# Kernel tuning notes

Measured on AMD Instinct MI355X. Metric: run time of the kernel, lower is better.

The kernel has to match this reference:

```python
import jax, jax.numpy as jnp
import numpy as np

N, F_IN, F_OUT, H = 4096, 128, 64, 8
NEG_SLOPE = 0.2

def leaky_relu(x):
    return jnp.where(x >= 0, x, NEG_SLOPE * x)

def setup_inputs() -> dict:
    key = jax.random.key(0)
    k = jax.random.split(key, 6)
    x = jax.random.normal(k[0], (N, F_IN), dtype=jnp.float32)
    conn = jax.random.uniform(k[1], (N, N)) < 0.1
    conn = conn | jnp.eye(N, dtype=bool)
    topology = jnp.where(conn, 0.0, -1e9).astype(jnp.float32)
    proj = jax.random.normal(k[2], (H, F_IN, F_OUT), dtype=jnp.float32) * (1.0 / np.sqrt(F_IN))
    score_src = jax.random.normal(k[3], (H, F_OUT), dtype=jnp.float32) * (1.0 / np.sqrt(F_OUT))
    score_dst = jax.random.normal(k[4], (H, F_OUT), dtype=jnp.float32) * (1.0 / np.sqrt(F_OUT))
    skip_w = jax.random.normal(k[5], (H * F_OUT, F_IN), dtype=jnp.float32) * (1.0 / np.sqrt(F_IN))
    return {"x": x, "topology": topology, "proj": proj,
            "score_src": score_src, "score_dst": score_dst, "skip_w": skip_w}

def reference(x, topology, proj, score_src, score_dst, skip_w):
    # dropout is identity at inference time
    # projected node features: [H, N, F_OUT]
    h = jnp.einsum('ni,hio->hno', x, proj)
    # additive attention scores (GAT): [H, N, 1] + [H, 1, N] -> [H, N, N]
    s_src = jnp.einsum('hno,ho->hn', h, score_src)
    s_dst = jnp.einsum('hno,ho->hn', h, score_dst)
    scores = leaky_relu(s_src[:, :, None] + s_dst[:, None, :])
    attn = jax.nn.softmax(scores + topology[None, :, :], axis=-1)  # [H, N, N]
    # aggregate neighbors, then transpose heads to [N, H, F_OUT]
    out = jnp.einsum('hij,hjo->iho', attn, h)
    # skip connection (F_OUT != F_IN -> projected skip)
    out = out + (x @ skip_w.T).reshape(N, H, F_OUT)
    # mean over heads (concat_heads=False), then LeakyReLU activation
    out = leaky_relu(jnp.mean(out, axis=1))  # [N, F_OUT]
    return out
```

## Files before the change

kernel.cpp:

```cpp
#include <hip/hip_runtime.h>
#include <hip/hip_bf16.h>

#define NN 4096
#define FIN 128
#define FOUT 64
#define NH 8
#define KS 4

typedef float f32x4 __attribute__((ext_vector_type(4)));
typedef _Float16 f16x8 __attribute__((ext_vector_type(8)));
typedef _Float16 h2 __attribute__((ext_vector_type(2)));
typedef unsigned long long u64;

static __device__ __forceinline__ h2 as_h2(unsigned u) { return __builtin_bit_cast(h2, u); }
static __device__ __forceinline__ unsigned as_u32(h2 v) { return __builtin_bit_cast(unsigned, v); }

static __device__ __forceinline__ u64 spread4(u64 x) {
    x = (x | (x << 24)) & 0x000000FF000000FFull;
    x = (x | (x << 12)) & 0x000F000F000F000Full;
    x = (x | (x << 6))  & 0x0303030303030303ull;
    x = (x | (x << 3))  & 0x1111111111111111ull;
    return x;
}

__global__ __launch_bounds__(256) void maskwc_kernel(
    const float* __restrict__ topo, u64* __restrict__ mb,
    const float* __restrict__ proj, const float* __restrict__ score_src,
    const float* __restrict__ score_dst, const float* __restrict__ skip_w,
    float* __restrict__ Wc) {
    const int tid = threadIdx.x;
    if (blockIdx.x < 2048) {
        const int wg = blockIdx.x * 4 + (tid >> 6);
        const int lane = tid & 63;
        const size_t base = (size_t)wg * 32;
        const float* tp = topo + base * 64 + lane * 4;
#pragma unroll
        for (int it = 0; it < 8; ++it) {
            float4 v = *(const float4*)(tp + it * 256);
            u64 b0 = __ballot(v.x > -0.5e9f);
            u64 b1 = __ballot(v.y > -0.5e9f);
            u64 b2 = __ballot(v.z > -0.5e9f);
            u64 b3 = __ballot(v.w > -0.5e9f);
            u64 wv[4];
#pragma unroll
            for (int g = 0; g < 4; ++g) {
                u64 x0 = spread4((b0 >> (16 * g)) & 0xFFFFu);
                u64 x1 = spread4((b1 >> (16 * g)) & 0xFFFFu);
                u64 x2 = spread4((b2 >> (16 * g)) & 0xFFFFu);
                u64 x3 = spread4((b3 >> (16 * g)) & 0xFFFFu);
                wv[g] = x0 | (x1 << 1) | (x2 << 2) | (x3 << 3);
            }
            if (lane == 0) {
                ulonglong2 s01; s01.x = wv[0]; s01.y = wv[1];
                ulonglong2 s23; s23.x = wv[2]; s23.y = wv[3];
                *(ulonglong2*)&mb[base + it * 4] = s01;
                *(ulonglong2*)&mb[base + it * 4 + 2] = s23;
            }
        }
        return;
    }
    int idx = (blockIdx.x - 2048) * 256 + tid;
    if (idx >= FIN * 80) return;
    int i = idx / 80, c = idx % 80;
    float v = 0.f;
    if (c < 16) {
        int h = c & 7;
        const float* w = (c < 8 ? score_src : score_dst) + h * FOUT;
        const float* p = proj + (size_t)h * FIN * FOUT + (size_t)i * FOUT;
        for (int f = 0; f < FOUT; ++f) v += p[f] * w[f];
    } else {
        int f = c - 16;
        for (int h = 0; h < NH; ++h) v += skip_w[(size_t)(h * FOUT + f) * FIN + i];
        v *= 0.125f;
    }
    Wc[i * 80 + c] = v;
}

__global__ __launch_bounds__(256) void scores_kernel(
    const float* __restrict__ x, const float* __restrict__ Wc,
    float* __restrict__ skipm, _Float16* __restrict__ Eh, _Float16* __restrict__ Fh,
    unsigned* __restrict__ Cc, _Float16* __restrict__ xb) {
    __shared__ float wcs[FIN][80];
    __shared__ float xs[16][FIN + 5];
    const int n0 = blockIdx.x * 16;
    const int tid = threadIdx.x;
    for (int i = tid; i < FIN * 80 / 4; i += 256)
        ((float4*)&wcs[0][0])[i] = ((const float4*)Wc)[i];
    const float4* xsrc = (const float4*)(x + (size_t)n0 * FIN);
    for (int i = tid; i < 16 * FIN / 4; i += 256) {
        int r = i >> 5, c4 = i & 31;
        *(float4*)&xs[r][c4 * 4] = xsrc[i];
    }
    __syncthreads();
    const int r = tid & 15;
    const int g = tid >> 4;
    float acc[4];
    float sa = 0.f;
#pragma unroll
    for (int j = 0; j < 4; ++j) acc[j] = 0.f;
#pragma unroll 4
    for (int i = 0; i < FIN; ++i) {
        float xv = xs[r][i];
        float4 p = *(float4*)&wcs[i][16 + g * 4];
        float qv = wcs[i][g];
        acc[0] += xv * p.x; acc[1] += xv * p.y; acc[2] += xv * p.z; acc[3] += xv * p.w;
        sa += xv * qv;
    }
    int n = n0 + r;
#pragma unroll
    for (int j = 0; j < 4; ++j) skipm[(size_t)n * FOUT + g * 4 + j] = acc[j];
    if (g < 8) {
        _Float16 c1 = (_Float16)(expf(sa) * 0.125f);
        _Float16 c2 = (_Float16)(expf(0.2f * sa) * 0.125f);
        unsigned short u1 = __builtin_bit_cast(unsigned short, c1);
        unsigned short u2 = __builtin_bit_cast(unsigned short, c2);
        Cc[(size_t)g * NN + n] = ((unsigned)u2 << 16) | (unsigned)u1;
    } else {
        int h = g - 8;
        Eh[(size_t)h * NN + n] = (_Float16)expf(sa);
        Fh[(size_t)h * NN + n] = (_Float16)expf(0.2f * sa);
    }
    {
        int row = tid >> 4, col0 = (tid & 15) * 8;
        const float* src = &xs[row][col0];
        f16x8 b0;
#pragma unroll
        for (int j = 0; j < 8; ++j) b0[j] = (_Float16)src[j];
        *(f16x8*)(xb + (size_t)(n0 + row) * FIN + col0) = b0;
    }
}

__global__ __launch_bounds__(256) void vt_kernel(
    const float* __restrict__ proj, const _Float16* __restrict__ xb,
    _Float16* __restrict__ Vt) {
    __shared__ _Float16 pT[FOUT][FIN + 8];
    const int tid = threadIdx.x;
    const int h = blockIdx.x >> 6;
    const int ng = blockIdx.x & 63;
    for (int idx = tid; idx < FIN * FOUT; idx += 256) {
        int i = idx >> 6, f = idx & 63;
        pT[f][i] = (_Float16)proj[(size_t)h * FIN * FOUT + idx];
    }
    __syncthreads();
    const int wave = tid >> 6, lane = tid & 63, q = lane >> 4, li = lane & 15;
    const int nb = ng * 64 + wave * 16;
    f32x4 acc[4];
#pragma unroll
    for (int n = 0; n < 4; ++n) acc[n] = (f32x4){0.f, 0.f, 0.f, 0.f};
#pragma unroll
    for (int kt = 0; kt < 4; ++kt) {
        f16x8 bfrag = *(const f16x8*)(xb + (size_t)(nb + li) * FIN + kt * 32 + q * 8);
#pragma unroll
        for (int ft = 0; ft < 4; ++ft) {
            f16x8 afrag = *(const f16x8*)&pT[ft * 16 + li][kt * 32 + q * 8];
            acc[ft] = __builtin_amdgcn_mfma_f32_16x16x32_f16(afrag, bfrag, acc[ft], 0, 0, 0);
        }
    }
#pragma unroll
    for (int ft = 0; ft < 4; ++ft)
#pragma unroll
        for (int reg = 0; reg < 4; ++reg)
            Vt[((size_t)h * FOUT + ft * 16 + q * 4 + reg) * NN + nb + li] = (_Float16)acc[ft][reg];
}

__attribute__((amdgpu_waves_per_eu(4)))
__global__ __launch_bounds__(256) void attn_kernel(
    const u64* __restrict__ maskbits, const _Float16* __restrict__ Vtg,
    const _Float16* __restrict__ Ehg, const _Float16* __restrict__ Fhg,
    const unsigned* __restrict__ Ccg,
    __hip_bfloat16* __restrict__ accP, float* __restrict__ rsP) {
    __shared__ u64 maskS[4][32][16];
    __shared__ char vbufB[24576];
    const int tid = threadIdx.x;
    const int w = tid >> 6;
    const int lane = tid & 63, q = lane >> 4, li = lane & 15;
    const int qt = blockIdx.x >> 5;
    const int ks = (blockIdx.x >> 3) & 3;
    const int h  = blockIdx.x & 7;
    const int row0 = qt * 128 + w * 32;
    const int kb0 = ks * 1024;

    const int r_ = lane >> 2;
    const int sg = ((lane & 3) - (r_ >> 1)) & 3;
    const _Float16* gsrc = Vtg + ((size_t)h * FOUT + w * 16 + r_) * NN + kb0 + sg * 8;
    const int rdoff = li * 64 + ((q + (li >> 1)) & 3) * 16;
    const _Float16* ehp = Ehg + (size_t)h * NN + kb0 + q * 8;
    const _Float16* fhp = Fhg + (size_t)h * NN + kb0 + q * 8;

#define DMA_TILE(BYTEOFF, OFF) \
    __builtin_amdgcn_global_load_lds( \
        (const __attribute__((address_space(1))) void*)(gsrc + (OFF)), \
        (__attribute__((address_space(3))) void*)&vbufB[(BYTEOFF) + w * 1024], 16, 0, 0)

    {
#pragma unroll
        for (int j = 0; j < 8; ++j) {
            int t = lane + j * 64;
            maskS[w][t >> 4][t & 15] =
                maskbits[(size_t)(row0 + (t >> 4)) * 64 + ks * 16 + (t & 15)];
        }
    }
    uint4 eA0 = *(const uint4*)(ehp);
    uint4 fA0 = *(const uint4*)(fhp);
    uint4 eA1 = *(const uint4*)(ehp + 32);
    uint4 fA1 = *(const uint4*)(fhp + 32);
    uint4 eB0, fB0, eB1, fB1;
    DMA_TILE(0, 0);
    DMA_TILE(4096, 32);

    h2 c1h[2], c2h[2];
#pragma unroll
    for (int rt = 0; rt < 2; ++rt) {
        unsigned cw = Ccg[(size_t)h * NN + row0 + rt * 16 + li];
        c1h[rt] = as_h2((cw << 16) | (cw & 0xffffu));
        c2h[rt] = as_h2((cw >> 16) | (cw & 0xffff0000u));
    }
    __syncthreads();

    f16x8 ones;
#pragma unroll
    for (int j = 0; j < 8; ++j) ones[j] = (_Float16)1.0f;

    f32x4 acc[2][4];
    f32x4 rsacc[2];
#pragma unroll
    for (int rt = 0; rt < 2; ++rt) {
#pragma unroll
        for (int n = 0; n < 4; ++n) acc[rt][n] = (f32x4){0.f, 0.f, 0.f, 0.f};
        rsacc[rt] = (f32x4){0.f, 0.f, 0.f, 0.f};
    }

    const u64* mp0 = &maskS[w][li][0];
    const u64* mp1 = &maskS[w][16 + li][0];
    u64 ma0 = mp0[0], ma1 = mp1[0];
    u64 mb0 = mp0[1], mb1 = mp1[1];

#define CHUNK_COMPUTE(CBYTE, EU, FU, PAR, MW0, MW1) do {                                      \
    f16x8 vf_[4];                                                                             \
    _Pragma("unroll")                                                                         \
    for (int n = 0; n < 4; ++n)                                                               \
        vf_[n] = *(const f16x8*)&vbufB[(CBYTE) + n * 1024 + rdoff];                           \
    unsigned ew_[4] = {EU.x, EU.y, EU.z, EU.w};                                               \
    unsigned fw_[4] = {FU.x, FU.y, FU.z, FU.w};                                               \
    _Pragma("unroll")                                                                         \
    for (int rt = 0; rt < 2; ++rt) {                                                          \
        u64 mw_ = rt ? (MW1) : (MW0);                                                         \
        unsigned mm_ = (unsigned)(mw_ >> ((PAR) * 32 + q * 8)) & 0xffu;                       \
        unsigned mlo_ = mm_ & 0xFu, mhi_ = mm_ >> 4;                                          \
        unsigned blo_ = (mlo_ | (mlo_ << 7) | (mlo_ << 14) | (mlo_ << 21)) & 0x01010101u;     \
        unsigned bhi_ = (mhi_ | (mhi_ << 7) | (mhi_ << 14) | (mhi_ << 21)) & 0x01010101u;     \
        blo_ = (blo_ << 8) - blo_;                                                            \
        bhi_ = (bhi_ << 8) - bhi_;                                                            \
        unsigned mk_[4] = {__builtin_amdgcn_perm(0u, blo_, 0x01010000u),                      \
                           __builtin_amdgcn_perm(0u, blo_, 0x03030202u),                      \
                           __builtin_amdgcn_perm(0u, bhi_, 0x01010000u),                      \
                           __builtin_amdgcn_perm(0u, bhi_, 0x03030202u)};                     \
        union { f16x8 v; unsigned u[4]; } pf_;                                                \
        _Pragma("unroll")                                                                     \
        for (int j2 = 0; j2 < 4; ++j2) {                                                      \
            h2 t_ = c1h[rt] * as_h2(ew_[j2]);                                                 \
            h2 u_ = c2h[rt] * as_h2(fw_[j2]);                                                 \
            h2 p_ = __builtin_elementwise_max(t_, u_);                                        \
            pf_.u[j2] = as_u32(p_) & mk_[j2];                                                 \
        }                                                                                     \
        rsacc[rt] = __builtin_amdgcn_mfma_f32_16x16x32_f16(pf_.v, ones, rsacc[rt], 0, 0, 0);  \
        _Pragma("unroll")                                                                     \
        for (int n = 0; n < 4; ++n)                                                           \
            acc[rt][n] = __builtin_amdgcn_mfma_f32_16x16x32_f16(pf_.v, vf_[n], acc[rt][n],    \
                                                                0, 0, 0);                     \
    }                                                                                         \
} while (0)

#define SBODY(CB, DB, EU0, FU0, EU1, FU1, EN0, FN0, EN1, FN1, EO0, EO1, MW0, MW1) do {        \
    EN0 = *(const uint4*)(ehp + (EO0));                                                       \
    FN0 = *(const uint4*)(fhp + (EO0));                                                       \
    EN1 = *(const uint4*)(ehp + (EO1));                                                       \
    FN1 = *(const uint4*)(fhp + (EO1));                                                       \
    asm volatile("" ::: "memory");                       \
    DMA_TILE((DB), (EO0));                                                                    \
    DMA_TILE((DB) + 4096, (EO1));                                                             \
    asm volatile("s_waitcnt vmcnt(6)" ::: "memory");                                          \
    __builtin_amdgcn_s_barrier();                                                             \
    __builtin_amdgcn_s_setprio(1);                                                            \
    CHUNK_COMPUTE((CB), EU0, FU0, 0, MW0, MW1);                                               \
    CHUNK_COMPUTE((CB) + 4096, EU1, FU1, 1, MW0, MW1);                                        \
    __builtin_amdgcn_s_setprio(0);                                                            \
} while (0)

    unsigned cb = 0, db = 8192;
#pragma unroll 1
    for (int i = 0; i < 8; ++i) {
        u64 na0 = mp0[2], na1 = mp1[2];
        u64 nb0 = mp0[3], nb1 = mp1[3];
        SBODY(cb, db, eA0, fA0, eA1, fA1, eB0, fB0, eB1, fB1, 64, 96, ma0, ma1);
        cb = db; db += 8192; if (db == 24576) db = 0;
        SBODY(cb, db, eB0, fB0, eB1, fB1, eA0, fA0, eA1, fA1, 128, 160, mb0, mb1);
        cb = db; db += 8192; if (db == 24576) db = 0;
        ma0 = na0; ma1 = na1; mb0 = nb0; mb1 = nb1;
        mp0 += 2; mp1 += 2;
        gsrc += 128; ehp += 128; fhp += 128;
    }
#undef SBODY
#undef CHUNK_COMPUTE
#undef DMA_TILE
    asm volatile("s_waitcnt vmcnt(0)" ::: "memory");

#pragma unroll
    for (int rt = 0; rt < 2; ++rt) {
        if (li == 0) {
#pragma unroll
            for (int reg = 0; reg < 4; ++reg)
                rsP[(size_t)(ks * NH + h) * NN + row0 + rt * 16 + q * 4 + reg] = rsacc[rt][reg];
        }
        __hip_bfloat16* ap = accP + ((size_t)(ks * NH + h) * NN + row0 + rt * 16) * 64;
#pragma unroll
        for (int n = 0; n < 4; ++n)
#pragma unroll
            for (int reg = 0; reg < 4; ++reg)
                ap[(q * 4 + reg) * 64 + n * 16 + li] = __float2bfloat16(acc[rt][n][reg]);
    }
}

__global__ __launch_bounds__(256) void combine_kernel(
    const __hip_bfloat16* __restrict__ accP, const float* __restrict__ rsP,
    float* __restrict__ out) {
    int idx = blockIdx.x * 256 + threadIdx.x;
    int row = idx >> 4, fg = (idx & 15) * 4;
    float s0 = 0.f, s1 = 0.f, s2 = 0.f, s3 = 0.f;
#pragma unroll 1
    for (int h = 0; h < NH; ++h) {
        float a0 = 0.f, a1 = 0.f, a2 = 0.f, a3 = 0.f, r = 0.f;
#pragma unroll
        for (int k = 0; k < KS; ++k) {
            const __hip_bfloat16* p = accP + ((size_t)(k * NH + h) * NN + row) * 64 + fg;
            uint2 v = *(const uint2*)p;
            a0 += __uint_as_float(v.x << 16);
            a1 += __uint_as_float(v.x & 0xffff0000u);
            a2 += __uint_as_float(v.y << 16);
            a3 += __uint_as_float(v.y & 0xffff0000u);
            r  += rsP[(size_t)(k * NH + h) * NN + row];
        }
        float ir = 1.0f / r;
        s0 += a0 * ir; s1 += a1 * ir; s2 += a2 * ir; s3 += a3 * ir;
    }
    float4 o = *(float4*)(out + (size_t)row * 64 + fg);
    float v0 = s0 * 0.125f + o.x, v1 = s1 * 0.125f + o.y;
    float v2 = s2 * 0.125f + o.z, v3 = s3 * 0.125f + o.w;
    o.x = fmaxf(v0, 0.2f * v0); o.y = fmaxf(v1, 0.2f * v1);
    o.z = fmaxf(v2, 0.2f * v2); o.w = fmaxf(v3, 0.2f * v3);
    *(float4*)(out + (size_t)row * 64 + fg) = o;
}

extern "C" void kernel_launch(void* const* d_in, const int* in_sizes, int n_in,
                              void* d_out, int out_size, void* d_ws, size_t ws_size,
                              hipStream_t stream) {
    (void)in_sizes; (void)n_in; (void)out_size; (void)ws_size;
    const float* x         = (const float*)d_in[0];
    const float* topology  = (const float*)d_in[1];
    const float* proj      = (const float*)d_in[2];
    const float* score_src = (const float*)d_in[3];
    const float* score_dst = (const float*)d_in[4];
    const float* skip_w    = (const float*)d_in[5];
    float* out = (float*)d_out;

    char* ws = (char*)d_ws;
    _Float16* xb   = (_Float16*)ws;
    _Float16* Vt   = (_Float16*)(ws + 1048576);
    _Float16* Eh   = (_Float16*)(ws + 5242880);
    _Float16* Fh   = (_Float16*)(ws + 5308416);
    unsigned* Cc   = (unsigned*)(ws + 5373952);
    float* Wc      = (float*)(ws + 5505024);
    u64* maskbits  = (u64*)(ws + 5545984);
    float* rsP     = (float*)(ws + 7643136);
    __hip_bfloat16* accP = (__hip_bfloat16*)(ws + 8167424);
    float* skipm = out;

    maskwc_kernel<<<2088, 256, 0, stream>>>(topology, maskbits, proj, score_src,
                                            score_dst, skip_w, Wc);
    scores_kernel<<<256, 256, 0, stream>>>(x, Wc, skipm, Eh, Fh, Cc, xb);
    vt_kernel<<<512, 256, 0, stream>>>(proj, xb, Vt);
    attn_kernel<<<1024, 256, 0, stream>>>(maskbits, Vt, Eh, Fh, Cc, accP, rsP);
    combine_kernel<<<256, 256, 0, stream>>>(accP, rsP, out);
}
```

Before: 187.5 us.

## Restructure attention pipeline to per-chunk barriers with 4-slot LDS ring

Changes the software pipeline from two-chunk super-steps over three 8KB buffers to single-chunk steps over a four-slot 4KB LDS ring. Each step prefetches only the next chunk's E/F vectors and DMAs the chunk two ahead, then waits and barriers. The s_setprio hints are dropped. The mask LDS rows are padded from 16 to 18 to reduce bank conflicts. This cuts register and LDS footprint and gives finer-grained overlap, at the cost of twice as many barriers per iteration.

```diff
diff --git a/kernel.cpp b/kernel.cpp
--- a/kernel.cpp
+++ b/kernel.cpp
@@ -169,8 +169,8 @@
     const _Float16* __restrict__ Ehg, const _Float16* __restrict__ Fhg,
     const unsigned* __restrict__ Ccg,
     __hip_bfloat16* __restrict__ accP, float* __restrict__ rsP) {
-    __shared__ u64 maskS[4][32][16];
-    __shared__ char vbufB[24576];
+    __shared__ u64 maskS[4][32][18];
+    __shared__ char vbuf[4][4096];
     const int tid = threadIdx.x;
     const int w = tid >> 6;
     const int lane = tid & 63, q = lane >> 4, li = lane & 15;
@@ -187,10 +187,10 @@
     const _Float16* ehp = Ehg + (size_t)h * NN + kb0 + q * 8;
     const _Float16* fhp = Fhg + (size_t)h * NN + kb0 + q * 8;
 
-#define DMA_TILE(BYTEOFF, OFF) \
+#define DMA_TILE(B, OFF) \
     __builtin_amdgcn_global_load_lds( \
         (const __attribute__((address_space(1))) void*)(gsrc + (OFF)), \
-        (__attribute__((address_space(3))) void*)&vbufB[(BYTEOFF) + w * 1024], 16, 0, 0)
+        (__attribute__((address_space(3))) void*)&vbuf[B][w * 1024], 16, 0, 0)
 
     {
 #pragma unroll
@@ -200,13 +200,11 @@
                 maskbits[(size_t)(row0 + (t >> 4)) * 64 + ks * 16 + (t & 15)];
         }
     }
-    uint4 eA0 = *(const uint4*)(ehp);
-    uint4 fA0 = *(const uint4*)(fhp);
-    uint4 eA1 = *(const uint4*)(ehp + 32);
-    uint4 fA1 = *(const uint4*)(fhp + 32);
-    uint4 eB0, fB0, eB1, fB1;
+    uint4 e0 = *(const uint4*)(ehp);
+    uint4 f0 = *(const uint4*)(fhp);
+    uint4 e1, f1;
     DMA_TILE(0, 0);
-    DMA_TILE(4096, 32);
+    DMA_TILE(1, 32);
 
     h2 c1h[2], c2h[2];
 #pragma unroll
@@ -235,17 +233,23 @@
     u64 ma0 = mp0[0], ma1 = mp1[0];
     u64 mb0 = mp0[1], mb1 = mp1[1];
 
-#define CHUNK_COMPUTE(CBYTE, EU, FU, PAR, MW0, MW1) do {                                      \
+#define BODY(K2, EU, FU, EN, FN, MW0, MW1) do {                                               \
+    EN = *(const uint4*)(ehp + ((K2) + 1) * 32);                                              \
+    FN = *(const uint4*)(fhp + ((K2) + 1) * 32);                                              \
+    asm volatile("" ::: "memory");                        \
+    DMA_TILE(((K2) + 2) & 3, ((K2) + 2) * 32);                                                \
+    asm volatile("s_waitcnt vmcnt(4)" ::: "memory");                                          \
+    __builtin_amdgcn_s_barrier();                                                             \
     f16x8 vf_[4];                                                                             \
     _Pragma("unroll")                                                                         \
     for (int n = 0; n < 4; ++n)                                                               \
-        vf_[n] = *(const f16x8*)&vbufB[(CBYTE) + n * 1024 + rdoff];                           \
+        vf_[n] = *(const f16x8*)&vbuf[K2][n * 1024 + rdoff];                                  \
     unsigned ew_[4] = {EU.x, EU.y, EU.z, EU.w};                                               \
     unsigned fw_[4] = {FU.x, FU.y, FU.z, FU.w};                                               \
     _Pragma("unroll")                                                                         \
     for (int rt = 0; rt < 2; ++rt) {                                                          \
         u64 mw_ = rt ? (MW1) : (MW0);                                                         \
-        unsigned mm_ = (unsigned)(mw_ >> ((PAR) * 32 + q * 8)) & 0xffu;                       \
+        unsigned mm_ = (unsigned)(mw_ >> (((K2) & 1) * 32 + q * 8)) & 0xffu;                  \
         unsigned mlo_ = mm_ & 0xFu, mhi_ = mm_ >> 4;                                          \
         unsigned blo_ = (mlo_ | (mlo_ << 7) | (mlo_ << 14) | (mlo_ << 21)) & 0x01010101u;     \
         unsigned bhi_ = (mhi_ | (mhi_ << 7) | (mhi_ << 14) | (mhi_ << 21)) & 0x01010101u;     \
@@ -271,38 +275,21 @@
     }                                                                                         \
 } while (0)
 
-#define SBODY(CB, DB, EU0, FU0, EU1, FU1, EN0, FN0, EN1, FN1, EO0, EO1, MW0, MW1) do {        \
-    EN0 = *(const uint4*)(ehp + (EO0));                                                       \
-    FN0 = *(const uint4*)(fhp + (EO0));                                                       \
-    EN1 = *(const uint4*)(ehp + (EO1));                                                       \
-    FN1 = *(const uint4*)(fhp + (EO1));                                                       \
-    asm volatile("" ::: "memory");                       \
-    DMA_TILE((DB), (EO0));                                                                    \
-    DMA_TILE((DB) + 4096, (EO1));                                                             \
-    asm volatile("s_waitcnt vmcnt(6)" ::: "memory");                                          \
-    __builtin_amdgcn_s_barrier();                                                             \
-    __builtin_amdgcn_s_setprio(1);                                                            \
-    CHUNK_COMPUTE((CB), EU0, FU0, 0, MW0, MW1);                                               \
-    CHUNK_COMPUTE((CB) + 4096, EU1, FU1, 1, MW0, MW1);                                        \
-    __builtin_amdgcn_s_setprio(0);                                                            \
-} while (0)
-
-    unsigned cb = 0, db = 8192;
 #pragma unroll 1
     for (int i = 0; i < 8; ++i) {
         u64 na0 = mp0[2], na1 = mp1[2];
         u64 nb0 = mp0[3], nb1 = mp1[3];
-        SBODY(cb, db, eA0, fA0, eA1, fA1, eB0, fB0, eB1, fB1, 64, 96, ma0, ma1);
-        cb = db; db += 8192; if (db == 24576) db = 0;
-        SBODY(cb, db, eB0, fB0, eB1, fB1, eA0, fA0, eA1, fA1, 128, 160, mb0, mb1);
-        cb = db; db += 8192; if (db == 24576) db = 0;
+        BODY(0, e0, f0, e1, f1, ma0, ma1);
+        BODY(1, e1, f1, e0, f0, ma0, ma1);
+        BODY(2, e0, f0, e1, f1, mb0, mb1);
+        BODY(3, e1, f1, e0, f0, mb0, mb1);
         ma0 = na0; ma1 = na1; mb0 = nb0; mb1 = nb1;
         mp0 += 2; mp1 += 2;
         gsrc += 128; ehp += 128; fhp += 128;
     }
-#undef SBODY
-#undef CHUNK_COMPUTE
+#undef BODY
 #undef DMA_TILE
+
     asm volatile("s_waitcnt vmcnt(0)" ::: "memory");
 
 #pragma unroll
```

Result: faster. 178.1 us, median of 2 (-5.0%).
